# Kernel optimization log

Hardware: AMD Instinct MI355X
Metric: run time of the kernel (lower is better)

## Reference

```python
import jax, jax.numpy as jnp
import numpy as np

N, E, F_IN, HID, HEADS, L, G = 20000, 200000, 20, 128, 4, 4, 32
NEG_SLOPE = 0.2


def setup_inputs() -> dict:
    key = jax.random.key(0)
    ks = jax.random.split(key, 12)
    s = 0.05
    x = jax.random.normal(ks[0], (N, F_IN), jnp.float32)
    edge_index = jax.random.randint(ks[1], (2, E), 0, N, jnp.int32)
    batch = jnp.sort(jax.random.randint(ks[2], (N,), 0, G, jnp.int32))
    W_in = jax.random.normal(ks[3], (F_IN, HID), jnp.float32) * s
    b_in = jnp.zeros((HID,), jnp.float32)
    gat_W = jax.random.normal(ks[4], (L, HID, HEADS * HID), jnp.float32) * s
    att_src = jax.random.normal(ks[5], (L, HEADS, HID), jnp.float32) * s
    att_dst = jax.random.normal(ks[6], (L, HEADS, HID), jnp.float32) * s
    gat_b = jnp.zeros((L, HID), jnp.float32)
    W1 = jax.random.normal(ks[7], (HID, HID // 2), jnp.float32) * s
    b1 = jnp.zeros((HID // 2,), jnp.float32)
    W2 = jax.random.normal(ks[8], (HID // 2, 64), jnp.float32) * s
    b2 = jnp.zeros((64,), jnp.float32)
    W3 = jax.random.normal(ks[9], (64, 32), jnp.float32) * s
    b3 = jnp.zeros((32,), jnp.float32)
    return dict(x=x, edge_index=edge_index, batch=batch, W_in=W_in, b_in=b_in,
                gat_W=gat_W, att_src=att_src, att_dst=att_dst, gat_b=gat_b,
                W1=W1, b1=b1, W2=W2, b2=b2, W3=W3, b3=b3)


def _gat_layer(x, src, dst, W, a_src, a_dst, b):
    # x: [N, HID]; W: [HID, HEADS*HID]; a_*: [HEADS, HID]
    xl = (x @ W).reshape(N, HEADS, HID)                      # [N, H, C]
    al_src = jnp.einsum('nhc,hc->nh', xl, a_src)             # [N, H]
    al_dst = jnp.einsum('nhc,hc->nh', xl, a_dst)             # [N, H]
    e = jax.nn.leaky_relu(al_src[src] + al_dst[dst], NEG_SLOPE)  # [Etot, H]
    # segment softmax over incoming edges of each dst node
    m = jax.ops.segment_max(e, dst, num_segments=N)          # [N, H]
    e = jnp.exp(e - m[dst])
    z = jax.ops.segment_sum(e, dst, num_segments=N)          # [N, H]
    alpha = e / (z[dst] + 1e-16)                             # [Etot, H]
    msg = xl[src] * alpha[:, :, None]                        # [Etot, H, C]
    out = jax.ops.segment_sum(msg, dst, num_segments=N)      # [N, H, C]
    return out.mean(axis=1) + b                              # concat=False: mean over heads


def reference(x, edge_index, batch, W_in, b_in, gat_W, att_src, att_dst, gat_b,
              W1, b1, W2, b2, W3, b3):
    # add self-loops (PyG GATConv default)
    loops = jnp.arange(N, dtype=edge_index.dtype)
    src = jnp.concatenate([edge_index[0], loops])
    dst = jnp.concatenate([edge_index[1], loops])
    h = jax.nn.relu(x @ W_in + b_in)
    for l in range(L):
        h = jax.nn.relu(_gat_layer(h, src, dst, gat_W[l], att_src[l], att_dst[l], gat_b[l])) + h
    # global mean pool per graph
    sums = jax.ops.segment_sum(h, batch, num_segments=G)     # [G, HID]
    cnt = jax.ops.segment_sum(jnp.ones((N,), h.dtype), batch, num_segments=G)
    g = sums / jnp.maximum(cnt, 1.0)[:, None]
    # output MLP (dropout is identity in eval mode)
    g = jax.nn.relu(g @ W1 + b1)
    g = jax.nn.relu(g @ W2 + b2)
    return g @ W3 + b3                                        # [G, 32]
```

## Files before the change

kernel.cpp:

```cpp
#include <hip/hip_runtime.h>

#define N_NODES 20000
#define N_PAD   20032
#define N_EDGES 200000
#define ETOT    (N_EDGES + N_NODES)
#define F_IN    20
#define HID     128
#define HEADS   4
#define FTOT    (HEADS * HID)
#define LAYERS  4
#define NGRAPH  32
#define NEG_SLOPE 0.2f

typedef __attribute__((ext_vector_type(8))) unsigned short ushortx8;
typedef __attribute__((ext_vector_type(8))) short short8;
typedef __attribute__((ext_vector_type(4))) float f32x4;

static __device__ __forceinline__ unsigned short f2bf(float f) {
    unsigned u = __float_as_uint(f);
    u += 0x7FFFu + ((u >> 16) & 1u);
    return (unsigned short)(u >> 16);
}
static __device__ __forceinline__ float bf2f(unsigned short s) {
    return __uint_as_float(((unsigned)s) << 16);
}


__global__ void k_hist(const int* __restrict__ ei, int* __restrict__ deg) {
    int i = blockIdx.x * blockDim.x + threadIdx.x;
    if (i >= ETOT) return;
    int d = (i < N_EDGES) ? ei[N_EDGES + i] : (i - N_EDGES);
    atomicAdd(&deg[d], 1);
}

__global__ __launch_bounds__(1024) void k_scan(const int* __restrict__ deg, int* __restrict__ off) {
    __shared__ int wsum[16];
    __shared__ int carry_s;
    int tid  = threadIdx.x;
    int lane = tid & 63, wv = tid >> 6;
    if (tid == 0) carry_s = 0;
    __syncthreads();
    for (int base = 0; base < N_NODES; base += 1024) {
        int idx = base + tid;
        int v = (idx < N_NODES) ? deg[idx] : 0;
        int x = v;
        #pragma unroll
        for (int s = 1; s < 64; s <<= 1) {
            int t = __shfl_up(x, s, 64);
            if (lane >= s) x += t;
        }
        if (lane == 63) wsum[wv] = x;
        __syncthreads();
        if (wv == 0) {
            int ws = (lane < 16) ? wsum[lane] : 0;
            #pragma unroll
            for (int s = 1; s < 16; s <<= 1) {
                int t = __shfl_up(ws, s, 64);
                if (lane >= s) ws += t;
            }
            if (lane < 16) wsum[lane] = ws;
        }
        __syncthreads();
        int wprev = (wv == 0) ? 0 : wsum[wv - 1];
        int incl  = carry_s + wprev + x;
        if (idx < N_NODES) off[idx] = incl - v;
        __syncthreads();
        if (tid == 1023) carry_s = incl;
        __syncthreads();
    }
    if (threadIdx.x == 0) off[N_NODES] = carry_s;
}

__global__ void k_scatter(const int* __restrict__ ei, const int* __restrict__ off,
                          int* __restrict__ cur, int* __restrict__ csr_src) {
    int i = blockIdx.x * blockDim.x + threadIdx.x;
    if (i >= ETOT) return;
    int s, d;
    if (i < N_EDGES) { s = ei[i]; d = ei[N_EDGES + i]; }
    else             { s = d = i - N_EDGES; }
    int pos = off[d] + atomicAdd(&cur[d], 1);
    csr_src[pos] = s;
}


__global__ void k_bounds(const int* __restrict__ batch, int* __restrict__ gstart) {
    int i = blockIdx.x * blockDim.x + threadIdx.x;
    if (i >= N_NODES) return;
    int b = batch[i];
    int prev = (i == 0) ? -1 : batch[i - 1];
    for (int g = prev + 1; g <= b; ++g) gstart[g] = i;
    if (i == N_NODES - 1) {
        for (int g = b + 1; g <= NGRAPH; ++g) gstart[g] = N_NODES;
    }
}


__global__ void k_wconv(const float* __restrict__ W, unsigned short* __restrict__ wswz) {
    int o = blockIdx.x * 256 + threadIdx.x;
    if (o >= LAYERS * 32 * 4 * 64 * 8) return;
    int e    = o & 7;
    int lane = (o >> 3) & 63;
    int kc   = (o >> 9) & 3;
    int cg   = (o >> 11) & 31;
    int l    = o >> 16;
    int k    = kc * 32 + (lane >> 4) * 8 + e;
    int col  = cg * 16 + (lane & 15);
    wswz[o] = f2bf(W[((size_t)l * HID + k) * FTOT + col]);
}


__global__ __launch_bounds__(256) void k_inproj(const float* __restrict__ x,
                                                const float* __restrict__ W,
                                                const float* __restrict__ b,
                                                float* __restrict__ h,
                                                unsigned short* __restrict__ hb) {
    __shared__ float xs[2][F_IN];
    int tid = threadIdx.x;
    int node0 = blockIdx.x * 2;
    if (tid < 2 * F_IN) {
        int r = tid / F_IN, k = tid % F_IN;
        int nd = node0 + r;
        xs[r][k] = (nd < N_NODES) ? x[nd * F_IN + k] : 0.f;
    }
    __syncthreads();
    int ln = tid >> 7;
    int c  = tid & 127;
    int node = node0 + ln;
    if (node >= N_NODES) return;
    float s = b[c];
    #pragma unroll
    for (int k = 0; k < F_IN; ++k) s += xs[ln][k] * W[k * HID + c];
    float r = fmaxf(s, 0.f);
    h[(size_t)node * HID + c] = r;
    hb[(size_t)node * HID + c] = f2bf(r);
}


__global__ __launch_bounds__(256) void k_gemm(const unsigned short* __restrict__ hb,
                                              const unsigned short* __restrict__ wswz,
                                              const float* __restrict__ asrc,
                                              const float* __restrict__ adst,
                                              unsigned short* __restrict__ xl,
                                              float* __restrict__ al_s,
                                              float* __restrict__ al_d) {
    int tid  = threadIdx.x;
    int lane = tid & 63;
    int w    = tid >> 6;
    int r0   = blockIdx.x * 64 + w * 16;
    int hd   = blockIdx.y;
    int arow = r0 + (lane & 15);
    const short8* ap = (const short8*)(hb + (size_t)arow * HID + (lane >> 4) * 8);
    const short8* bp = (const short8*)wswz;
    short8 a[4];
    #pragma unroll
    for (int kc = 0; kc < 4; ++kc) a[kc] = ap[kc * 4];
    f32x4 acc[8];
    #pragma unroll
    for (int ct = 0; ct < 8; ++ct) {
        f32x4 c = {0.f, 0.f, 0.f, 0.f};
        int cg = hd * 8 + ct;
        #pragma unroll
        for (int kc = 0; kc < 4; ++kc) {
            short8 b = bp[(cg * 4 + kc) * 64 + lane];
            c = __builtin_amdgcn_mfma_f32_16x16x32_bf16(a[kc], b, c, 0, 0, 0);
        }
        acc[ct] = c;
    }
    int ocol = lane & 15;
    int orow = r0 + (lane >> 4) * 4;
    float vs[4] = {}, vd[4] = {};
    #pragma unroll
    for (int ct = 0; ct < 8; ++ct) {
        int colg = hd * 128 + ct * 16 + ocol;
        float as = asrc[colg], ad = adst[colg];
        #pragma unroll
        for (int r = 0; r < 4; ++r) {
            vs[r] += acc[ct][r] * as;
            vd[r] += acc[ct][r] * ad;
            int row = orow + r;
            if (row < N_NODES) xl[(size_t)row * FTOT + colg] = f2bf(acc[ct][r]);
        }
    }
    #pragma unroll
    for (int msk = 1; msk < 16; msk <<= 1) {
        #pragma unroll
        for (int r = 0; r < 4; ++r) {
            vs[r] += __shfl_xor(vs[r], msk, 64);
            vd[r] += __shfl_xor(vd[r], msk, 64);
        }
    }
    if (ocol == 0) {
        #pragma unroll
        for (int r = 0; r < 4; ++r) {
            int row = orow + r;
            if (row < N_NODES) {
                al_s[row * HEADS + hd] = vs[r];
                al_d[row * HEADS + hd] = vd[r];
            }
        }
    }
}


__global__ __launch_bounds__(256) void k_agg(const unsigned short* __restrict__ xl,
                                             const float* __restrict__ al_s,
                                             const float* __restrict__ al_d,
                                             const int* __restrict__ csr_off,
                                             const int* __restrict__ csr_src,
                                             const float* __restrict__ bias,
                                             float* __restrict__ h,
                                             unsigned short* __restrict__ hb) {
    __shared__ float buf[2][HID];
    int tid   = threadIdx.x;
    int lane  = tid & 63;
    int w     = tid >> 6;
    int nip   = w >> 1;
    int chalf = w & 1;
    int node  = blockIdx.x * 2 + nip;
    int hh    = chalf * 2 + (lane >> 5);
    int e0 = csr_off[node], e1 = csr_off[node + 1];
    float ald = al_d[node * HEADS + hh];

    float m = -1e30f, z = 0.f;
    for (int e = e0 + (lane & 31); e < e1; e += 32) {
        int s = csr_src[e];
        float ev = al_s[s * HEADS + hh] + ald;
        ev = ev > 0.f ? ev : NEG_SLOPE * ev;
        float mn = fmaxf(m, ev);
        z = z * __expf(m - mn) + __expf(ev - mn);
        m = mn;
    }
    #pragma unroll
    for (int msk = 1; msk < 32; msk <<= 1) {
        float m2 = __shfl_xor(m, msk, 64);
        float z2 = __shfl_xor(z, msk, 64);
        float mn = fmaxf(m, m2);
        z = z * __expf(m - mn) + z2 * __expf(m2 - mn);
        m = mn;
    }
    float zinv = 1.f / (z + 1e-16f);

    float acc0 = 0.f, acc1 = 0.f, acc2 = 0.f, acc3 = 0.f;
    const unsigned short* xbase = xl + chalf * 256 + lane * 4;
    int e = e0;
    for (; e + 1 < e1; e += 2) {
        int s0 = csr_src[e], s1 = csr_src[e + 1];
        float ev0 = al_s[s0 * HEADS + hh] + ald;
        float ev1 = al_s[s1 * HEADS + hh] + ald;
        ushort4 v0 = *(const ushort4*)(xbase + (size_t)s0 * FTOT);
        ushort4 v1 = *(const ushort4*)(xbase + (size_t)s1 * FTOT);
        ev0 = ev0 > 0.f ? ev0 : NEG_SLOPE * ev0;
        ev1 = ev1 > 0.f ? ev1 : NEG_SLOPE * ev1;
        float a0 = __expf(ev0 - m) * zinv;
        float a1 = __expf(ev1 - m) * zinv;
        acc0 += a0 * bf2f(v0.x) + a1 * bf2f(v1.x);
        acc1 += a0 * bf2f(v0.y) + a1 * bf2f(v1.y);
        acc2 += a0 * bf2f(v0.z) + a1 * bf2f(v1.z);
        acc3 += a0 * bf2f(v0.w) + a1 * bf2f(v1.w);
    }
    if (e < e1) {
        int s0 = csr_src[e];
        float ev0 = al_s[s0 * HEADS + hh] + ald;
        ushort4 v0 = *(const ushort4*)(xbase + (size_t)s0 * FTOT);
        ev0 = ev0 > 0.f ? ev0 : NEG_SLOPE * ev0;
        float a0 = __expf(ev0 - m) * zinv;
        acc0 += a0 * bf2f(v0.x);
        acc1 += a0 * bf2f(v0.y);
        acc2 += a0 * bf2f(v0.z);
        acc3 += a0 * bf2f(v0.w);
    }
    acc0 += __shfl_xor(acc0, 32, 64);
    acc1 += __shfl_xor(acc1, 32, 64);
    acc2 += __shfl_xor(acc2, 32, 64);
    acc3 += __shfl_xor(acc3, 32, 64);
    if (chalf == 1 && lane < 32) {
        int c = lane * 4;
        buf[nip][c]     = acc0;
        buf[nip][c + 1] = acc1;
        buf[nip][c + 2] = acc2;
        buf[nip][c + 3] = acc3;
    }
    __syncthreads();
    if (chalf == 0 && lane < 32) {
        int c = lane * 4;
        float4 hv = *(const float4*)(h + (size_t)node * HID + c);
        float4 bb = *(const float4*)(bias + c);
        float o0 = fmaxf((acc0 + buf[nip][c])     * 0.25f + bb.x, 0.f) + hv.x;
        float o1 = fmaxf((acc1 + buf[nip][c + 1]) * 0.25f + bb.y, 0.f) + hv.y;
        float o2 = fmaxf((acc2 + buf[nip][c + 2]) * 0.25f + bb.z, 0.f) + hv.z;
        float o3 = fmaxf((acc3 + buf[nip][c + 3]) * 0.25f + bb.w, 0.f) + hv.w;
        *(float4*)(h + (size_t)node * HID + c) = make_float4(o0, o1, o2, o3);
        ushort4 hv16;
        hv16.x = f2bf(o0); hv16.y = f2bf(o1); hv16.z = f2bf(o2); hv16.w = f2bf(o3);
        *(ushort4*)(hb + (size_t)node * HID + c) = hv16;
    }
}


__global__ __launch_bounds__(128) void k_pool(const float* __restrict__ h,
                                              const int* __restrict__ gstart,
                                              float* __restrict__ pooled) {
    int g = blockIdx.y;
    int slice = blockIdx.x;
    int tid = threadIdx.x;
    int start = gstart[g];
    int cnt   = gstart[g + 1] - start;
    int per = (cnt + 31) / 32;
    int r0 = slice * per, r1 = min(r0 + per, cnt);
    if (r0 >= r1) return;
    float s0 = 0.f, s1 = 0.f, s2 = 0.f, s3 = 0.f;
    int r = r0;
    for (; r + 3 < r1; r += 4) {
        s0 += h[(size_t)(start + r)     * HID + tid];
        s1 += h[(size_t)(start + r + 1) * HID + tid];
        s2 += h[(size_t)(start + r + 2) * HID + tid];
        s3 += h[(size_t)(start + r + 3) * HID + tid];
    }
    for (; r < r1; ++r) s0 += h[(size_t)(start + r) * HID + tid];
    atomicAdd(&pooled[g * HID + tid], (s0 + s1) + (s2 + s3));
}

__global__ __launch_bounds__(256) void k_mlp(const float* __restrict__ pooled,
                                             const int* __restrict__ gstart,
                                             const float* __restrict__ W1, const float* __restrict__ b1,
                                             const float* __restrict__ W2, const float* __restrict__ b2,
                                             const float* __restrict__ W3, const float* __restrict__ b3,
                                             float* __restrict__ out) {
    int gr = blockIdx.x;
    __shared__ float g[HID];
    __shared__ float part[4][64];
    __shared__ float t1[64], t2[64];
    int tid = threadIdx.x;
    if (tid < HID) {
        float inv = 1.f / fmaxf((float)(gstart[gr + 1] - gstart[gr]), 1.f);
        g[tid] = pooled[gr * HID + tid] * inv;
    }
    __syncthreads();
    {
        int c = tid & 63, q = tid >> 6;
        float s = 0.f;
        #pragma unroll 8
        for (int k = q * 32; k < q * 32 + 32; ++k) s += g[k] * W1[k * 64 + c];
        part[q][c] = s;
        __syncthreads();
        if (tid < 64) t1[tid] = fmaxf(part[0][tid] + part[1][tid] + part[2][tid] + part[3][tid] + b1[tid], 0.f);
        __syncthreads();
    }
    {
        int c = tid & 63, q = tid >> 6;
        float s = 0.f;
        #pragma unroll 8
        for (int k = q * 16; k < q * 16 + 16; ++k) s += t1[k] * W2[k * 64 + c];
        part[q][c] = s;
        __syncthreads();
        if (tid < 64) t2[tid] = fmaxf(part[0][tid] + part[1][tid] + part[2][tid] + part[3][tid] + b2[tid], 0.f);
        __syncthreads();
    }
    {
        int c = tid & 31, q = tid >> 5;
        float s = 0.f;
        #pragma unroll 8
        for (int k = q * 8; k < q * 8 + 8; ++k) s += t2[k] * W3[k * 32 + c];
        float* pf = &part[0][0];
        pf[q * 32 + c] = s;
        __syncthreads();
        if (tid < 32) {
            float r = b3[tid];
            #pragma unroll
            for (int q2 = 0; q2 < 8; ++q2) r += pf[q2 * 32 + tid];
            out[gr * 32 + tid] = r;
        }
    }
}


extern "C" void kernel_launch(void* const* d_in, const int* in_sizes, int n_in,
                              void* d_out, int out_size, void* d_ws, size_t ws_size,
                              hipStream_t stream) {
    const float* x       = (const float*)d_in[0];
    const int*   ei      = (const int*)d_in[1];
    const int*   batch   = (const int*)d_in[2];
    const float* W_in    = (const float*)d_in[3];
    const float* b_in    = (const float*)d_in[4];
    const float* gat_W   = (const float*)d_in[5];
    const float* att_src = (const float*)d_in[6];
    const float* att_dst = (const float*)d_in[7];
    const float* gat_b   = (const float*)d_in[8];
    const float* W1 = (const float*)d_in[9];
    const float* b1 = (const float*)d_in[10];
    const float* W2 = (const float*)d_in[11];
    const float* b2 = (const float*)d_in[12];
    const float* W3 = (const float*)d_in[13];
    const float* b3 = (const float*)d_in[14];
    float* out = (float*)d_out;

    char* ws = (char*)d_ws;
    size_t o = 0;
    auto alloc = [&](size_t nbytes) -> void* {
        void* p = ws + o;
        o += (nbytes + 255) & ~(size_t)255;
        return p;
    };
    int* deg      = (int*)alloc((size_t)2 * N_NODES * 4);
    int* cur      = deg + N_NODES;
    int* gstart   = (int*)alloc((size_t)(NGRAPH + 1) * 4);
    float* pooled = (float*)alloc((size_t)NGRAPH * HID * 4);
    int* csr_off  = (int*)alloc((size_t)(N_NODES + 1) * 4);
    int* csr_src  = (int*)alloc((size_t)ETOT * 4);
    float* h      = (float*)alloc((size_t)N_NODES * HID * 4);
    unsigned short* hb   = (unsigned short*)alloc((size_t)N_PAD * HID * 2);
    unsigned short* xl   = (unsigned short*)alloc((size_t)N_NODES * FTOT * 2);
    unsigned short* wswz = (unsigned short*)alloc((size_t)LAYERS * HID * FTOT * 2);
    float* al_s   = (float*)alloc((size_t)N_NODES * HEADS * 4);
    float* al_d   = (float*)alloc((size_t)N_NODES * HEADS * 4);

    hipMemsetAsync(deg, 0, (size_t)2 * N_NODES * 4, stream);
    hipMemsetAsync(pooled, 0, (size_t)NGRAPH * HID * 4, stream);

    k_hist<<<(ETOT + 255) / 256, 256, 0, stream>>>(ei, deg);
    k_scan<<<1, 1024, 0, stream>>>(deg, csr_off);
    k_scatter<<<(ETOT + 255) / 256, 256, 0, stream>>>(ei, csr_off, cur, csr_src);
    k_bounds<<<(N_NODES + 255) / 256, 256, 0, stream>>>(batch, gstart);
    k_wconv<<<(LAYERS * 32 * 4 * 64 * 8) / 256, 256, 0, stream>>>(gat_W, wswz);

    k_inproj<<<(N_NODES + 1) / 2, 256, 0, stream>>>(x, W_in, b_in, h, hb);

    for (int l = 0; l < LAYERS; ++l) {
        k_gemm<<<dim3(N_PAD / 64, HEADS), 256, 0, stream>>>(
            hb, wswz + (size_t)l * HID * FTOT,
            att_src + (size_t)l * HEADS * HID, att_dst + (size_t)l * HEADS * HID,
            xl, al_s, al_d);
        k_agg<<<N_NODES / 2, 256, 0, stream>>>(
            xl, al_s, al_d, csr_off, csr_src, gat_b + (size_t)l * HID, h, hb);
    }

    k_pool<<<dim3(32, NGRAPH), 128, 0, stream>>>(h, gstart, pooled);
    k_mlp<<<NGRAPH, 256, 0, stream>>>(pooled, gstart, W1, b1, W2, b2, W3, b3, out);
}
```

Before: 403.2 us.

## Restructure GAT aggregation to one wave per node with cached attention weights

The aggregation kernel now gives each destination node a single 64-lane wave instead of two waves. Each lane handles 8 contiguous bf16 features, loaded as 16-byte vectors, and 16 lanes cover each head. The softmax pass computes the edge scores once, then stores the exponentials in shared memory for up to 64 edges, so the gather pass no longer reloads al_s or recomputes exp. Heads are reduced with shuffles rather than a cross-wave shared-memory exchange. In exchange, fewer lanes work on the softmax pass, and nodes with more than 64 incoming edges fall back to recomputing the scores.

```diff
diff --git a/kernel.cpp b/kernel.cpp
--- a/kernel.cpp
+++ b/kernel.cpp
@@ -11,6 +11,7 @@
 #define LAYERS  4
 #define NGRAPH  32
 #define NEG_SLOPE 0.2f
+#define DEG_CAP 64
 
 typedef __attribute__((ext_vector_type(8))) unsigned short ushortx8;
 typedef __attribute__((ext_vector_type(8))) short short8;
@@ -210,28 +211,57 @@
                                              const float* __restrict__ bias,
                                              float* __restrict__ h,
                                              unsigned short* __restrict__ hb) {
-    __shared__ float buf[2][HID];
-    int tid   = threadIdx.x;
-    int lane  = tid & 63;
-    int w     = tid >> 6;
-    int nip   = w >> 1;
-    int chalf = w & 1;
-    int node  = blockIdx.x * 2 + nip;
-    int hh    = chalf * 2 + (lane >> 5);
+    __shared__ float alds[4][DEG_CAP][HEADS];
+    int tid  = threadIdx.x;
+    int lane = tid & 63;
+    int wid  = tid >> 6;
+    int node = blockIdx.x * 4 + wid;
+    if (node >= N_NODES) return;
+    int hh = lane >> 4;
+    int el = lane & 15;
     int e0 = csr_off[node], e1 = csr_off[node + 1];
+    int deg = e1 - e0;
     float ald = al_d[node * HEADS + hh];
 
-    float m = -1e30f, z = 0.f;
-    for (int e = e0 + (lane & 31); e < e1; e += 32) {
-        int s = csr_src[e];
-        float ev = al_s[s * HEADS + hh] + ald;
-        ev = ev > 0.f ? ev : NEG_SLOPE * ev;
-        float mn = fmaxf(m, ev);
-        z = z * __expf(m - mn) + __expf(ev - mn);
+    float ev0 = -1e30f, ev1 = -1e30f, ev2 = -1e30f, ev3 = -1e30f;
+    {
+        if (el < deg) {
+            int s = csr_src[e0 + el];
+            float e = al_s[s * HEADS + hh] + ald;
+            ev0 = e > 0.f ? e : NEG_SLOPE * e;
+        }
+        if (el + 16 < deg) {
+            int s = csr_src[e0 + el + 16];
+            float e = al_s[s * HEADS + hh] + ald;
+            ev1 = e > 0.f ? e : NEG_SLOPE * e;
+        }
+        if (el + 32 < deg) {
+            int s = csr_src[e0 + el + 32];
+            float e = al_s[s * HEADS + hh] + ald;
+            ev2 = e > 0.f ? e : NEG_SLOPE * e;
+        }
+        if (el + 48 < deg) {
+            int s = csr_src[e0 + el + 48];
+            float e = al_s[s * HEADS + hh] + ald;
+            ev3 = e > 0.f ? e : NEG_SLOPE * e;
+        }
+    }
+    float m = fmaxf(fmaxf(ev0, ev1), fmaxf(ev2, ev3));
+    float z = 0.f;
+    if (el      < deg) z += __expf(ev0 - m);
+    if (el + 16 < deg) z += __expf(ev1 - m);
+    if (el + 32 < deg) z += __expf(ev2 - m);
+    if (el + 48 < deg) z += __expf(ev3 - m);
+    for (int i = el + DEG_CAP; i < deg; i += 16) {
+        int s = csr_src[e0 + i];
+        float e = al_s[s * HEADS + hh] + ald;
+        e = e > 0.f ? e : NEG_SLOPE * e;
+        float mn = fmaxf(m, e);
+        z = z * __expf(m - mn) + __expf(e - mn);
         m = mn;
     }
     #pragma unroll
-    for (int msk = 1; msk < 32; msk <<= 1) {
+    for (int msk = 1; msk < 16; msk <<= 1) {
         float m2 = __shfl_xor(m, msk, 64);
         float z2 = __shfl_xor(z, msk, 64);
         float mn = fmaxf(m, m2);
@@ -239,60 +269,68 @@
         m = mn;
     }
     float zinv = 1.f / (z + 1e-16f);
-
-    float acc0 = 0.f, acc1 = 0.f, acc2 = 0.f, acc3 = 0.f;
-    const unsigned short* xbase = xl + chalf * 256 + lane * 4;
-    int e = e0;
-    for (; e + 1 < e1; e += 2) {
-        int s0 = csr_src[e], s1 = csr_src[e + 1];
-        float ev0 = al_s[s0 * HEADS + hh] + ald;
-        float ev1 = al_s[s1 * HEADS + hh] + ald;
-        ushort4 v0 = *(const ushort4*)(xbase + (size_t)s0 * FTOT);
-        ushort4 v1 = *(const ushort4*)(xbase + (size_t)s1 * FTOT);
-        ev0 = ev0 > 0.f ? ev0 : NEG_SLOPE * ev0;
-        ev1 = ev1 > 0.f ? ev1 : NEG_SLOPE * ev1;
-        float a0 = __expf(ev0 - m) * zinv;
-        float a1 = __expf(ev1 - m) * zinv;
-        acc0 += a0 * bf2f(v0.x) + a1 * bf2f(v1.x);
-        acc1 += a0 * bf2f(v0.y) + a1 * bf2f(v1.y);
-        acc2 += a0 * bf2f(v0.z) + a1 * bf2f(v1.z);
-        acc3 += a0 * bf2f(v0.w) + a1 * bf2f(v1.w);
-    }
-    if (e < e1) {
-        int s0 = csr_src[e];
-        float ev0 = al_s[s0 * HEADS + hh] + ald;
-        ushort4 v0 = *(const ushort4*)(xbase + (size_t)s0 * FTOT);
-        ev0 = ev0 > 0.f ? ev0 : NEG_SLOPE * ev0;
-        float a0 = __expf(ev0 - m) * zinv;
-        acc0 += a0 * bf2f(v0.x);
-        acc1 += a0 * bf2f(v0.y);
-        acc2 += a0 * bf2f(v0.z);
-        acc3 += a0 * bf2f(v0.w);
-    }
-    acc0 += __shfl_xor(acc0, 32, 64);
-    acc1 += __shfl_xor(acc1, 32, 64);
-    acc2 += __shfl_xor(acc2, 32, 64);
-    acc3 += __shfl_xor(acc3, 32, 64);
-    if (chalf == 1 && lane < 32) {
-        int c = lane * 4;
-        buf[nip][c]     = acc0;
-        buf[nip][c + 1] = acc1;
-        buf[nip][c + 2] = acc2;
-        buf[nip][c + 3] = acc3;
-    }
+    if (el      < deg) alds[wid][el     ][hh] = __expf(ev0 - m);
+    if (el + 16 < deg) alds[wid][el + 16][hh] = __expf(ev1 - m);
+    if (el + 32 < deg) alds[wid][el + 32][hh] = __expf(ev2 - m);
+    if (el + 48 < deg) alds[wid][el + 48][hh] = __expf(ev3 - m);
     __syncthreads();
-    if (chalf == 0 && lane < 32) {
-        int c = lane * 4;
-        float4 hv = *(const float4*)(h + (size_t)node * HID + c);
-        float4 bb = *(const float4*)(bias + c);
-        float o0 = fmaxf((acc0 + buf[nip][c])     * 0.25f + bb.x, 0.f) + hv.x;
-        float o1 = fmaxf((acc1 + buf[nip][c + 1]) * 0.25f + bb.y, 0.f) + hv.y;
-        float o2 = fmaxf((acc2 + buf[nip][c + 2]) * 0.25f + bb.z, 0.f) + hv.z;
-        float o3 = fmaxf((acc3 + buf[nip][c + 3]) * 0.25f + bb.w, 0.f) + hv.w;
-        *(float4*)(h + (size_t)node * HID + c) = make_float4(o0, o1, o2, o3);
-        ushort4 hv16;
-        hv16.x = f2bf(o0); hv16.y = f2bf(o1); hv16.z = f2bf(o2); hv16.w = f2bf(o3);
-        *(ushort4*)(hb + (size_t)node * HID + c) = hv16;
+
+    float acc[8] = {};
+    const unsigned short* xbase = xl + lane * 8;
+    int dcap = deg < DEG_CAP ? deg : DEG_CAP;
+    int i = 0;
+    for (; i + 1 < dcap; i += 2) {
+        int s0 = csr_src[e0 + i];
+        int s1 = csr_src[e0 + i + 1];
+        float a0 = alds[wid][i][hh];
+        float a1 = alds[wid][i + 1][hh];
+        ushortx8 v0 = *(const ushortx8*)(xbase + (size_t)s0 * FTOT);
+        ushortx8 v1 = *(const ushortx8*)(xbase + (size_t)s1 * FTOT);
+        #pragma unroll
+        for (int j = 0; j < 8; ++j) acc[j] += a0 * bf2f(v0[j]) + a1 * bf2f(v1[j]);
+    }
+    if (i < dcap) {
+        int s0 = csr_src[e0 + i];
+        float a0 = alds[wid][i][hh];
+        ushortx8 v0 = *(const ushortx8*)(xbase + (size_t)s0 * FTOT);
+        #pragma unroll
+        for (int j = 0; j < 8; ++j) acc[j] += a0 * bf2f(v0[j]);
+    }
+    for (int t = DEG_CAP; t < deg; ++t) {
+        int s0 = csr_src[e0 + t];
+        float e = al_s[s0 * HEADS + hh] + ald;
+        e = e > 0.f ? e : NEG_SLOPE * e;
+        float a0 = __expf(e - m);
+        ushortx8 v0 = *(const ushortx8*)(xbase + (size_t)s0 * FTOT);
+        #pragma unroll
+        for (int j = 0; j < 8; ++j) acc[j] += a0 * bf2f(v0[j]);
+    }
+    #pragma unroll
+    for (int j = 0; j < 8; ++j) {
+        acc[j] *= zinv;
+        acc[j] += __shfl_xor(acc[j], 16, 64);
+        acc[j] += __shfl_xor(acc[j], 32, 64);
+    }
+    if (lane < 16) {
+        int c = lane * 8;
+        float4 hv0 = *(const float4*)(h + (size_t)node * HID + c);
+        float4 hv1 = *(const float4*)(h + (size_t)node * HID + c + 4);
+        float4 b0 = *(const float4*)(bias + c);
+        float4 b1 = *(const float4*)(bias + c + 4);
+        float o0 = fmaxf(acc[0] * 0.25f + b0.x, 0.f) + hv0.x;
+        float o1 = fmaxf(acc[1] * 0.25f + b0.y, 0.f) + hv0.y;
+        float o2 = fmaxf(acc[2] * 0.25f + b0.z, 0.f) + hv0.z;
+        float o3 = fmaxf(acc[3] * 0.25f + b0.w, 0.f) + hv0.w;
+        float o4 = fmaxf(acc[4] * 0.25f + b1.x, 0.f) + hv1.x;
+        float o5 = fmaxf(acc[5] * 0.25f + b1.y, 0.f) + hv1.y;
+        float o6 = fmaxf(acc[6] * 0.25f + b1.z, 0.f) + hv1.z;
+        float o7 = fmaxf(acc[7] * 0.25f + b1.w, 0.f) + hv1.w;
+        *(float4*)(h + (size_t)node * HID + c)     = make_float4(o0, o1, o2, o3);
+        *(float4*)(h + (size_t)node * HID + c + 4) = make_float4(o4, o5, o6, o7);
+        ushortx8 hv;
+        hv[0] = f2bf(o0); hv[1] = f2bf(o1); hv[2] = f2bf(o2); hv[3] = f2bf(o3);
+        hv[4] = f2bf(o4); hv[5] = f2bf(o5); hv[6] = f2bf(o6); hv[7] = f2bf(o7);
+        *(ushortx8*)(hb + (size_t)node * HID + c) = hv;
     }
 }
 
@@ -430,7 +468,7 @@
             hb, wswz + (size_t)l * HID * FTOT,
             att_src + (size_t)l * HEADS * HID, att_dst + (size_t)l * HEADS * HID,
             xl, al_s, al_d);
-        k_agg<<<N_NODES / 2, 256, 0, stream>>>(
+        k_agg<<<(N_NODES + 3) / 4, 256, 0, stream>>>(
             xl, al_s, al_d, csr_off, csr_src, gat_b + (size_t)l * HID, h, hb);
     }
 
```

Result: faster. 366.5 us (-9.1%).
